# Kernel optimization log

Measured on AMD Instinct MI355X. Metric: run time of the kernel, lower is better.

Reference implementation:

```python
import jax, jax.numpy as jnp
import numpy as np

KH = KW = 3  # deform conv kernel
EPS = 1e-12  # F.normalize eps


def _deform_sample(img, u, v):
    """Flow-guided deformable sampling: bilinear gather of img at each of the
    9 kernel offsets shifted by the per-pixel flow (u=dx, v=dy).
    img: [B,C,H,W]; u,v: [B,1,H,W] -> returns [B,C,9,H,W]."""
    B, C, H, W = img.shape
    ky, kx = jnp.meshgrid(jnp.arange(KH) - 1, jnp.arange(KW) - 1, indexing='ij')
    ky = ky.reshape(1, 9, 1, 1).astype(img.dtype)
    kx = kx.reshape(1, 9, 1, 1).astype(img.dtype)
    iy = jnp.arange(H, dtype=img.dtype).reshape(1, 1, H, 1)
    ix = jnp.arange(W, dtype=img.dtype).reshape(1, 1, 1, W)
    py = iy + ky + v  # [B,9,H,W]
    px = ix + kx + u
    y0 = jnp.floor(py); x0 = jnp.floor(px)
    wy = py - y0; wx = px - x0  # bilinear weights
    y0i = y0.astype(jnp.int32); x0i = x0.astype(jnp.int32)
    flat = img.reshape(B, C, H * W)

    def gather(yi, xi):
        valid = ((yi >= 0) & (yi < H) & (xi >= 0) & (xi < W)).astype(img.dtype)
        idx = jnp.clip(yi, 0, H - 1) * W + jnp.clip(xi, 0, W - 1)  # [B,9,H,W]
        g = jax.vmap(lambda f, i: jnp.take(f, i.reshape(-1), axis=1))(flat, idx)
        return g.reshape(B, C, 9, H, W) * valid[:, None]

    s = (gather(y0i, x0i) * ((1 - wy) * (1 - wx))[:, None]
         + gather(y0i, x0i + 1) * ((1 - wy) * wx)[:, None]
         + gather(y0i + 1, x0i) * (wy * (1 - wx))[:, None]
         + gather(y0i + 1, x0i + 1) * (wy * wx)[:, None])
    return s


def setup_inputs() -> dict:
    key = jax.random.key(0)
    k1, k2, k3, k4, k5 = jax.random.split(key, 5)
    B, C, H, W = 2, 64, 256, 256
    num_heads = 4
    clone = jax.random.normal(k1, (B, C, H, W), dtype=jnp.float32)
    x = jax.random.normal(k2, (B, C, H * W), dtype=jnp.float32)
    u = jax.random.normal(k3, (B, 1, H, W), dtype=jnp.float32)
    v = jax.random.normal(k4, (B, 1, H, W), dtype=jnp.float32)
    weight = jax.random.normal(k5, (C, C, KH, KW), dtype=jnp.float32) * 0.05
    temperature = jnp.ones((num_heads, 1, 1), dtype=jnp.float32)
    return {"clone": clone, "x": x, "u": u, "v": v,
            "weight": weight, "temperature": temperature}


def reference(clone, x, u, v, weight, temperature):
    # deformable conv: bilinear gather then contract over (in_ch, kernel)
    s = _deform_sample(clone, u, v)                      # [B,C,9,H,W]
    w = weight.reshape(weight.shape[0], weight.shape[1], 9)
    conv = jnp.einsum('bckhw,ock->bohw', s, w)           # [B,C,H,W]
    B, C, H, W = conv.shape
    head = temperature.shape[0]
    kv = conv.reshape(B, head, C // head, H * W)          # k = v = deform output
    q = x.reshape(B, head, C // head, H * W)
    qn = q / jnp.maximum(jnp.linalg.norm(q, axis=-1, keepdims=True), EPS)
    kn = kv / jnp.maximum(jnp.linalg.norm(kv, axis=-1, keepdims=True), EPS)
    attn = jnp.einsum('bhcs,bhds->bhcd', qn, kn) * temperature  # [B,h,c,c]
    attn = jax.nn.softmax(attn, axis=-1)
    out = jnp.einsum('bhcd,bhds->bhcs', attn, kv)
    return out.reshape(B, C, H * W)
```

## Files before the change

### kernel.cpp

```cpp
#include <hip/hip_runtime.h>

typedef __bf16 bf16;
typedef __bf16 bf16x4 __attribute__((ext_vector_type(4)));
typedef __bf16 bf16x8 __attribute__((ext_vector_type(8)));
typedef float  f32x4  __attribute__((ext_vector_type(4)));

#define HH 256
#define WW 256
#define NB 2
#define NC 64
#define NS 65536
#define EX 258
#define NHEAD 4
#define DH 16

#define OFF_CEXT   0ul
#define OFF_KV     17040384ul
#define OFF_WPK    33817600ul
#define OFF_ACC    33891328ul

__global__ void k0w(const float* __restrict__ wgt, bf16* __restrict__ wpk,
                    float* __restrict__ accums) {
    int t = blockIdx.x * 256 + threadIdx.x;
    if (t < 9 * 2 * 4 * 64) {
        int L   = t & 63;
        int mtg = (t >> 6) & 3;
        int kc  = (t >> 8) & 1;
        int tap = t >> 9;
        int o  = mtg * 16 + (L & 15);
        int cb = kc * 32 + (L >> 4) * 8;
        bf16x8 vv;
        #pragma unroll
        for (int j = 0; j < 8; j++)
            vv[j] = (bf16)wgt[(o * 64 + (cb + j)) * 9 + tap];
        *(bf16x8*)(wpk + t * 8) = vv;
    }
    int z = t - 9 * 2 * 4 * 64;
    if (z >= 0 && z < 2304) accums[z] = 0.0f;
}

__global__ __launch_bounds__(256, 2) void k1_conv(const float* __restrict__ clone,
                                                  const bf16* __restrict__ wpk,
                                                  bf16* __restrict__ cext) {
    const int Xt = blockIdx.x;
    const int Yt = blockIdx.y;
    const int b  = blockIdx.z;
    const int t  = threadIdx.x;
    const int L  = t & 63;
    const int wv = t >> 6;
    const int mpair = wv >> 1;
    const int npair = wv & 1;

    extern __shared__ bf16 tile[];

    bf16x8 afrag[2][9][2];
    #pragma unroll
    for (int mt = 0; mt < 2; mt++)
        #pragma unroll
        for (int tap = 0; tap < 9; tap++)
            #pragma unroll
            for (int kc = 0; kc < 2; kc++) {
                int idx = ((tap * 2 + kc) * 4 + (mpair * 2 + mt)) * 64 + L;
                afrag[mt][tap][kc] = *(const bf16x8*)(wpk + idx * 8);
            }

    for (int u = t; u < 2176; u += 256) {
        int xq = u % 17;
        int rc = u / 17;
        int cg = rc & 15;
        int r  = rc >> 4;
        int y  = Yt * 6 - 2 + r;
        int xg0 = Xt * 64 - 4 + xq * 4;
        int c0 = cg * 4;
        f32x4 f[4];
        bool yin = (y >= 0) && (y < HH);
        if (yin && xg0 >= 0 && xg0 + 3 < WW) {
            #pragma unroll
            for (int i = 0; i < 4; i++)
                f[i] = *(const f32x4*)(clone + ((size_t)(b * NC + c0 + i) * HH + y) * WW + xg0);
        } else {
            #pragma unroll
            for (int i = 0; i < 4; i++)
                #pragma unroll
                for (int e = 0; e < 4; e++) {
                    int xg = xg0 + e;
                    f[i][e] = (yin && xg >= 0 && xg < WW)
                            ? clone[((size_t)(b * NC + c0 + i) * HH + y) * WW + xg] : 0.0f;
                }
        }
        #pragma unroll
        for (int e = 0; e < 4; e++) {
            bf16x4 h;
            #pragma unroll
            for (int i = 0; i < 4; i++) h[i] = (bf16)f[i][e];
            *(bf16x4*)(tile + (r * 68 + xq * 4 + e) * 72 + c0) = h;
        }
    }
    __syncthreads();

    const f32x4 zero4 = {0.0f, 0.0f, 0.0f, 0.0f};
    for (int Yi = 0; Yi < 6; Yi++) {
        f32x4 acc[2][2];
        acc[0][0] = zero4; acc[0][1] = zero4; acc[1][0] = zero4; acc[1][1] = zero4;
        #pragma unroll
        for (int tap = 0; tap < 9; tap++) {
            const int ky = tap / 3 - 1;
            const int kx = tap % 3 - 1;
            const int r = Yi + 1 + ky;
            #pragma unroll
            for (int kc = 0; kc < 2; kc++) {
                const int cb = kc * 32 + (L >> 4) * 8;
                #pragma unroll
                for (int nt = 0; nt < 2; nt++) {
                    const int col = npair * 32 + nt * 16 + (L & 15) + kx + 3;
                    bf16x8 bfrag = *(const bf16x8*)(tile + (r * 68 + col) * 72 + cb);
                    #pragma unroll
                    for (int mt = 0; mt < 2; mt++)
                        acc[mt][nt] = __builtin_amdgcn_mfma_f32_16x16x32_bf16(
                            afrag[mt][tap][kc], bfrag, acc[mt][nt], 0, 0, 0);
                }
            }
        }
        int Yp = Yt * 6 + Yi;
        #pragma unroll
        for (int mt = 0; mt < 2; mt++)
            #pragma unroll
            for (int nt = 0; nt < 2; nt++) {
                int Xp = Xt * 64 + npair * 32 + nt * 16 + (L & 15);
                if (Xp < EX) {
                    int o = mpair * 32 + mt * 16 + (L >> 4) * 4;
                    bf16x4 st;
                    #pragma unroll
                    for (int rg = 0; rg < 4; rg++) st[rg] = (bf16)acc[mt][nt][rg];
                    *(bf16x4*)(cext + ((((size_t)b * EX + Yp) * EX + Xp) << 6) + o) = st;
                }
            }
    }
}

__global__ __launch_bounds__(256) void k2_gather(const float* __restrict__ uu,
                                                 const float* __restrict__ vv,
                                                 const bf16* __restrict__ cext,
                                                 bf16* __restrict__ kv) {
    const int tx = blockIdx.x;
    const int ty = blockIdx.y;
    const int b  = blockIdx.z;
    const int t  = threadIdx.x;
    const int px = t & 31, py = t >> 5;
    const int hw = (ty * 8 + py) * 256 + tx * 32 + px;
    const int idx = b * NS + hw;
    const int hy = hw >> 8;
    const int wx = hw & 255;
    float fv = vv[idx];
    float fu = uu[idx];
    float py_f = (float)hy + fv;
    float px_f = (float)wx + fu;
    float fy = floorf(py_f);
    float fx = floorf(px_f);
    float ay = py_f - fy;
    float ax = px_f - fx;
    int ys = (int)fy + 1;
    int xs = (int)fx + 1;
    float w00 = (1.0f - ay) * (1.0f - ax);
    float w01 = (1.0f - ay) * ax;
    float w10 = ay * (1.0f - ax);
    float w11 = ay * ax;
    bool y0i = (ys >= 0) && (ys < EX);
    bool y1i = (ys + 1 >= 0) && (ys + 1 < EX);
    bool x0i = (xs >= 0) && (xs < EX);
    bool x1i = (xs + 1 >= 0) && (xs + 1 < EX);
    if (!y0i) { w00 = 0.0f; w01 = 0.0f; }
    if (!y1i) { w10 = 0.0f; w11 = 0.0f; }
    if (!x0i) { w00 = 0.0f; w10 = 0.0f; }
    if (!x1i) { w01 = 0.0f; w11 = 0.0f; }
    int y0c = ys < 0 ? 0 : (ys > EX - 1 ? EX - 1 : ys);
    int y1c = ys + 1 < 0 ? 0 : (ys + 1 > EX - 1 ? EX - 1 : ys + 1);
    int x0c = xs < 0 ? 0 : (xs > EX - 1 ? EX - 1 : xs);
    int x1c = xs + 1 < 0 ? 0 : (xs + 1 > EX - 1 ? EX - 1 : xs + 1);
    const bf16* pb = cext + (((size_t)b * EX * EX) << 6);
    size_t i00 = ((size_t)(y0c * EX + x0c)) << 6;
    size_t i01 = ((size_t)(y0c * EX + x1c)) << 6;
    size_t i10 = ((size_t)(y1c * EX + x0c)) << 6;
    size_t i11 = ((size_t)(y1c * EX + x1c)) << 6;
    bf16* kvp = kv + (((size_t)(b * NC)) << 16) + hw;
    #pragma unroll
    for (int ck = 0; ck < 8; ck++) {
        int c0 = ck * 8;
        bf16x8 c00 = *(const bf16x8*)(pb + i00 + c0);
        bf16x8 c01 = *(const bf16x8*)(pb + i01 + c0);
        bf16x8 c10 = *(const bf16x8*)(pb + i10 + c0);
        bf16x8 c11 = *(const bf16x8*)(pb + i11 + c0);
        #pragma unroll
        for (int j = 0; j < 8; j++) {
            float val = w00 * (float)c00[j] + w01 * (float)c01[j]
                      + w10 * (float)c10[j] + w11 * (float)c11[j];
            kvp[((size_t)(c0 + j)) << 16] = (bf16)val;
        }
    }
}

__global__ __launch_bounds__(256) void k3_dots(const float* __restrict__ x,
                                               const bf16* __restrict__ kv,
                                               float* __restrict__ dots,
                                               float* __restrict__ qss,
                                               float* __restrict__ kss) {
    const int ch = blockIdx.x;
    const int h  = blockIdx.y;
    const int b  = blockIdx.z;
    const int t  = threadIdx.x;
    const int L  = t & 63;
    const int wv = t >> 6;
    const int row = L & 15;
    const int kg  = L >> 4;
    const float* qb = x + ((size_t)(b * NC + h * DH + row)) * NS;
    const bf16*  kb = kv + (((size_t)(b * NC + h * DH + row)) << 16);
    f32x4 acc = {0.0f, 0.0f, 0.0f, 0.0f};
    float qp = 0.0f, kp = 0.0f;
    const int s0 = ch * 512 + wv * 128 + kg * 8;
    #pragma unroll
    for (int it = 0; it < 4; it++) {
        int s = s0 + it * 32;
        f32x4 q0 = *(const f32x4*)(qb + s);
        f32x4 q1 = *(const f32x4*)(qb + s + 4);
        bf16x8 ka = *(const bf16x8*)(kb + s);
        bf16x8 qa;
        #pragma unroll
        for (int j = 0; j < 4; j++) {
            qa[j]     = (bf16)q0[j];
            qa[j + 4] = (bf16)q1[j];
        }
        qp += q0[0]*q0[0] + q0[1]*q0[1] + q0[2]*q0[2] + q0[3]*q0[3]
            + q1[0]*q1[0] + q1[1]*q1[1] + q1[2]*q1[2] + q1[3]*q1[3];
        #pragma unroll
        for (int j = 0; j < 8; j++) {
            float kf = (float)ka[j];
            kp += kf * kf;
        }
        acc = __builtin_amdgcn_mfma_f32_16x16x32_bf16(qa, ka, acc, 0, 0, 0);
    }
    __shared__ float ldsD[256];
    __shared__ float ldsQ[16];
    __shared__ float ldsK[16];
    ldsD[t] = 0.0f;
    if (t < 16) { ldsQ[t] = 0.0f; ldsK[t] = 0.0f; }
    __syncthreads();
    #pragma unroll
    for (int rg = 0; rg < 4; rg++)
        atomicAdd(&ldsD[(kg * 4 + rg) * 16 + row], acc[rg]);
    atomicAdd(&ldsQ[row], qp);
    atomicAdd(&ldsK[row], kp);
    __syncthreads();
    const int bh = b * NHEAD + h;
    atomicAdd(&dots[bh * 256 + t], ldsD[t]);
    if (t < 16) {
        atomicAdd(&qss[bh * 16 + t], ldsQ[t]);
        atomicAdd(&kss[bh * 16 + t], ldsK[t]);
    }
}

__global__ __launch_bounds__(256) void k5_out(const bf16* __restrict__ kv,
                                              const float* __restrict__ dots,
                                              const float* __restrict__ qss,
                                              const float* __restrict__ kss,
                                              const float* __restrict__ temp,
                                              float* __restrict__ out) {
    const int ci = blockIdx.x;
    const int h  = blockIdx.y;
    const int b  = blockIdx.z;
    const int t  = threadIdx.x;
    const int bh = b * NHEAD + h;
    __shared__ float l[256];
    __shared__ float a[256];
    {
        int i = t >> 4, j = t & 15;
        float qn = fmaxf(sqrtf(qss[bh * 16 + i]), 1e-12f);
        float kn = fmaxf(sqrtf(kss[bh * 16 + j]), 1e-12f);
        float logit = dots[bh * 256 + t] / (qn * kn) * temp[h];
        l[t] = logit;
        __syncthreads();
        float mx = -1e30f;
        #pragma unroll
        for (int jj = 0; jj < 16; jj++) mx = fmaxf(mx, l[i * 16 + jj]);
        float sum = 0.0f;
        #pragma unroll
        for (int jj = 0; jj < 16; jj++) sum += expf(l[i * 16 + jj] - mx);
        a[t] = expf(logit - mx) / sum;
        __syncthreads();
    }
    const int s = (ci * 256 + t) * 4;
    const bf16* kvb = kv + (((size_t)(b * NC + h * DH)) << 16) + s;
    f32x4 kf[16];
    #pragma unroll
    for (int j = 0; j < 16; j++) {
        bf16x4 kk = *(const bf16x4*)(kvb + ((size_t)j << 16));
        #pragma unroll
        for (int e = 0; e < 4; e++) kf[j][e] = (float)kk[e];
    }
    float* ob = out + ((size_t)(b * NC + h * DH)) * NS + s;
    #pragma unroll
    for (int i = 0; i < 16; i++) {
        f32x4 o = {0.0f, 0.0f, 0.0f, 0.0f};
        #pragma unroll
        for (int j = 0; j < 16; j++)
            o += a[i * 16 + j] * kf[j];
        *(f32x4*)(ob + (size_t)i * NS) = o;
    }
}

extern "C" void kernel_launch(void* const* d_in, const int* in_sizes, int n_in,
                              void* d_out, int out_size, void* d_ws, size_t ws_size,
                              hipStream_t stream) {
    const float* clone = (const float*)d_in[0];
    const float* x     = (const float*)d_in[1];
    const float* u     = (const float*)d_in[2];
    const float* v     = (const float*)d_in[3];
    const float* wgt   = (const float*)d_in[4];
    const float* temp  = (const float*)d_in[5];
    float* out = (float*)d_out;

    char* ws = (char*)d_ws;
    bf16*  cext   = (bf16*) (ws + OFF_CEXT);
    bf16*  kv     = (bf16*) (ws + OFF_KV);
    bf16*  wpk    = (bf16*) (ws + OFF_WPK);
    float* accums = (float*)(ws + OFF_ACC);
    float* dots = accums;
    float* qss  = accums + 2048;
    float* kss  = accums + 2048 + 128;

    static bool attr_set = false;
    if (!attr_set) {
        hipFuncSetAttribute((const void*)k1_conv,
                            hipFuncAttributeMaxDynamicSharedMemorySize, 78336);
        attr_set = true;
    }

    k0w<<<27, 256, 0, stream>>>(wgt, wpk, accums);
    k1_conv<<<dim3(5, 43, 2), 256, 78336, stream>>>(clone, wpk, cext);
    k2_gather<<<dim3(8, 32, 2), 256, 0, stream>>>(u, v, cext, kv);
    k3_dots<<<dim3(128, 4, 2), 256, 0, stream>>>(x, kv, dots, qss, kss);
    k5_out<<<dim3(64, 4, 2), 256, 0, stream>>>(kv, dots, qss, kss, temp, out);
}
```

Before: 161.7 us.

## Fuse deform gather with q·k dot reduction and stripe global accumulators

Merges the gather kernel and the dots kernel. Each block computes 128 pixels of kv, keeps them in a shared tile and runs the per-head q·k MFMA reduction directly from it, so the separate k3 pass no longer re-reads kv from global memory. Global atomics are spread over 8 accumulator stripes to reduce contention, and k5 sums the stripes. The conv kernel also skips MFMAs for column tiles that lie entirely past the valid extent. In exchange it adds more global atomics per block, since the LDS pre-reduction is gone, and the LDS tile read uses a strided pattern.

```diff
diff --git a/kernel.cpp b/kernel.cpp
--- a/kernel.cpp
+++ b/kernel.cpp
@@ -13,6 +13,8 @@
 #define EX 258
 #define NHEAD 4
 #define DH 16
+#define NSTRIPE 8
+#define ACCSZ 2304
 
 #define OFF_CEXT   0ul
 #define OFF_KV     17040384ul
@@ -36,7 +38,7 @@
         *(bf16x8*)(wpk + t * 8) = vv;
     }
     int z = t - 9 * 2 * 4 * 64;
-    if (z >= 0 && z < 2304) accums[z] = 0.0f;
+    if (z >= 0 && z < NSTRIPE * ACCSZ) accums[z] = 0.0f;
 }
 
 __global__ __launch_bounds__(256, 2) void k1_conv(const float* __restrict__ clone,
@@ -98,6 +100,7 @@
     }
     __syncthreads();
 
+    const int nbase = Xt * 64 + npair * 32;
     const f32x4 zero4 = {0.0f, 0.0f, 0.0f, 0.0f};
     for (int Yi = 0; Yi < 6; Yi++) {
         f32x4 acc[2][2];
@@ -112,12 +115,14 @@
                 const int cb = kc * 32 + (L >> 4) * 8;
                 #pragma unroll
                 for (int nt = 0; nt < 2; nt++) {
-                    const int col = npair * 32 + nt * 16 + (L & 15) + kx + 3;
-                    bf16x8 bfrag = *(const bf16x8*)(tile + (r * 68 + col) * 72 + cb);
-                    #pragma unroll
-                    for (int mt = 0; mt < 2; mt++)
-                        acc[mt][nt] = __builtin_amdgcn_mfma_f32_16x16x32_bf16(
-                            afrag[mt][tap][kc], bfrag, acc[mt][nt], 0, 0, 0);
+                    if (nbase + nt * 16 < EX) {
+                        const int col = npair * 32 + nt * 16 + (L & 15) + kx + 3;
+                        bf16x8 bfrag = *(const bf16x8*)(tile + (r * 68 + col) * 72 + cb);
+                        #pragma unroll
+                        for (int mt = 0; mt < 2; mt++)
+                            acc[mt][nt] = __builtin_amdgcn_mfma_f32_16x16x32_bf16(
+                                afrag[mt][tap][kc], bfrag, acc[mt][nt], 0, 0, 0);
+                    }
                 }
             }
         }
@@ -138,19 +143,25 @@
     }
 }
 
-__global__ __launch_bounds__(256) void k2_gather(const float* __restrict__ uu,
-                                                 const float* __restrict__ vv,
-                                                 const bf16* __restrict__ cext,
-                                                 bf16* __restrict__ kv) {
-    const int tx = blockIdx.x;
-    const int ty = blockIdx.y;
+__global__ __launch_bounds__(256) void k2_gd(const float* __restrict__ uu,
+                                             const float* __restrict__ vv,
+                                             const float* __restrict__ x,
+                                             const bf16* __restrict__ cext,
+                                             bf16* __restrict__ kv,
+                                             float* __restrict__ accums) {
+    const int bx = blockIdx.x;
     const int b  = blockIdx.z;
-    const int t  = threadIdx.x;
-    const int px = t & 31, py = t >> 5;
-    const int hw = (ty * 8 + py) * 256 + tx * 32 + px;
+    const int strip = (bx & 7) * 64 + (bx >> 3);
+    const int t = threadIdx.x;
+    const int px = t >> 1;
+    const int half = t & 1;
+    const int hw = strip * 128 + px;
     const int idx = b * NS + hw;
     const int hy = hw >> 8;
     const int wx = hw & 255;
+
+    __shared__ bf16 tile[128][68];
+
     float fv = vv[idx];
     float fu = uu[idx];
     float py_f = (float)hy + fv;
@@ -182,53 +193,50 @@
     size_t i01 = ((size_t)(y0c * EX + x1c)) << 6;
     size_t i10 = ((size_t)(y1c * EX + x0c)) << 6;
     size_t i11 = ((size_t)(y1c * EX + x1c)) << 6;
-    bf16* kvp = kv + (((size_t)(b * NC)) << 16) + hw;
-    #pragma unroll
-    for (int ck = 0; ck < 8; ck++) {
-        int c0 = ck * 8;
-        bf16x8 c00 = *(const bf16x8*)(pb + i00 + c0);
-        bf16x8 c01 = *(const bf16x8*)(pb + i01 + c0);
-        bf16x8 c10 = *(const bf16x8*)(pb + i10 + c0);
-        bf16x8 c11 = *(const bf16x8*)(pb + i11 + c0);
+    const int c0 = half * 32;
+    bf16* kvp = kv + (((size_t)(b * NC + c0)) << 16) + hw;
+    #pragma unroll
+    for (int g = 0; g < 4; g++) {
+        int cg = c0 + g * 8;
+        bf16x8 c00 = *(const bf16x8*)(pb + i00 + cg);
+        bf16x8 c01 = *(const bf16x8*)(pb + i01 + cg);
+        bf16x8 c10 = *(const bf16x8*)(pb + i10 + cg);
+        bf16x8 c11 = *(const bf16x8*)(pb + i11 + cg);
+        bf16x4 lo, hi;
         #pragma unroll
         for (int j = 0; j < 8; j++) {
             float val = w00 * (float)c00[j] + w01 * (float)c01[j]
                       + w10 * (float)c10[j] + w11 * (float)c11[j];
-            kvp[((size_t)(c0 + j)) << 16] = (bf16)val;
-        }
-    }
-}
-
-__global__ __launch_bounds__(256) void k3_dots(const float* __restrict__ x,
-                                               const bf16* __restrict__ kv,
-                                               float* __restrict__ dots,
-                                               float* __restrict__ qss,
-                                               float* __restrict__ kss) {
-    const int ch = blockIdx.x;
-    const int h  = blockIdx.y;
-    const int b  = blockIdx.z;
-    const int t  = threadIdx.x;
+            bf16 hv = (bf16)val;
+            if (j < 4) lo[j] = hv; else hi[j - 4] = hv;
+            kvp[((size_t)(g * 8 + j)) << 16] = hv;
+        }
+        *(bf16x4*)(&tile[px][c0 + g * 8])     = lo;
+        *(bf16x4*)(&tile[px][c0 + g * 8 + 4]) = hi;
+    }
+    __syncthreads();
+
     const int L  = t & 63;
-    const int wv = t >> 6;
+    const int h  = t >> 6;
     const int row = L & 15;
     const int kg  = L >> 4;
-    const float* qb = x + ((size_t)(b * NC + h * DH + row)) * NS;
-    const bf16*  kb = kv + (((size_t)(b * NC + h * DH + row)) << 16);
+    const int bh = b * NHEAD + h;
+    const float* qb = x + ((size_t)(b * NC + h * DH + row)) * NS + strip * 128;
     f32x4 acc = {0.0f, 0.0f, 0.0f, 0.0f};
     float qp = 0.0f, kp = 0.0f;
-    const int s0 = ch * 512 + wv * 128 + kg * 8;
     #pragma unroll
     for (int it = 0; it < 4; it++) {
-        int s = s0 + it * 32;
+        const int s = it * 32 + kg * 8;
         f32x4 q0 = *(const f32x4*)(qb + s);
         f32x4 q1 = *(const f32x4*)(qb + s + 4);
-        bf16x8 ka = *(const bf16x8*)(kb + s);
-        bf16x8 qa;
+        bf16x8 qa, ka;
         #pragma unroll
         for (int j = 0; j < 4; j++) {
             qa[j]     = (bf16)q0[j];
             qa[j + 4] = (bf16)q1[j];
         }
+        #pragma unroll
+        for (int j = 0; j < 8; j++) ka[j] = tile[s + j][h * DH + row];
         qp += q0[0]*q0[0] + q0[1]*q0[1] + q0[2]*q0[2] + q0[3]*q0[3]
             + q1[0]*q1[0] + q1[1]*q1[1] + q1[2]*q1[2] + q1[3]*q1[3];
         #pragma unroll
@@ -238,30 +246,20 @@
         }
         acc = __builtin_amdgcn_mfma_f32_16x16x32_bf16(qa, ka, acc, 0, 0, 0);
     }
-    __shared__ float ldsD[256];
-    __shared__ float ldsQ[16];
-    __shared__ float ldsK[16];
-    ldsD[t] = 0.0f;
-    if (t < 16) { ldsQ[t] = 0.0f; ldsK[t] = 0.0f; }
-    __syncthreads();
+    float* astripe = accums + (bx & 7) * ACCSZ;
     #pragma unroll
     for (int rg = 0; rg < 4; rg++)
-        atomicAdd(&ldsD[(kg * 4 + rg) * 16 + row], acc[rg]);
-    atomicAdd(&ldsQ[row], qp);
-    atomicAdd(&ldsK[row], kp);
-    __syncthreads();
-    const int bh = b * NHEAD + h;
-    atomicAdd(&dots[bh * 256 + t], ldsD[t]);
-    if (t < 16) {
-        atomicAdd(&qss[bh * 16 + t], ldsQ[t]);
-        atomicAdd(&kss[bh * 16 + t], ldsK[t]);
+        atomicAdd(astripe + bh * 256 + (kg * 4 + rg) * 16 + row, acc[rg]);
+    qp += __shfl_xor(qp, 16); qp += __shfl_xor(qp, 32);
+    kp += __shfl_xor(kp, 16); kp += __shfl_xor(kp, 32);
+    if (kg == 0) {
+        atomicAdd(astripe + 2048 + bh * 16 + row, qp);
+        atomicAdd(astripe + 2176 + bh * 16 + row, kp);
     }
 }
 
 __global__ __launch_bounds__(256) void k5_out(const bf16* __restrict__ kv,
-                                              const float* __restrict__ dots,
-                                              const float* __restrict__ qss,
-                                              const float* __restrict__ kss,
+                                              const float* __restrict__ accums,
                                               const float* __restrict__ temp,
                                               float* __restrict__ out) {
     const int ci = blockIdx.x;
@@ -273,9 +271,16 @@
     __shared__ float a[256];
     {
         int i = t >> 4, j = t & 15;
-        float qn = fmaxf(sqrtf(qss[bh * 16 + i]), 1e-12f);
-        float kn = fmaxf(sqrtf(kss[bh * 16 + j]), 1e-12f);
-        float logit = dots[bh * 256 + t] / (qn * kn) * temp[h];
+        float dsum = 0.0f, q2 = 0.0f, k2 = 0.0f;
+        #pragma unroll
+        for (int st = 0; st < NSTRIPE; st++) {
+            dsum += accums[st * ACCSZ + bh * 256 + t];
+            q2   += accums[st * ACCSZ + 2048 + bh * 16 + i];
+            k2   += accums[st * ACCSZ + 2176 + bh * 16 + j];
+        }
+        float qn = fmaxf(sqrtf(q2), 1e-12f);
+        float kn = fmaxf(sqrtf(k2), 1e-12f);
+        float logit = dsum / (qn * kn) * temp[h];
         l[t] = logit;
         __syncthreads();
         float mx = -1e30f;
@@ -323,9 +328,6 @@
     bf16*  kv     = (bf16*) (ws + OFF_KV);
     bf16*  wpk    = (bf16*) (ws + OFF_WPK);
     float* accums = (float*)(ws + OFF_ACC);
-    float* dots = accums;
-    float* qss  = accums + 2048;
-    float* kss  = accums + 2048 + 128;
 
     static bool attr_set = false;
     if (!attr_set) {
@@ -334,9 +336,8 @@
         attr_set = true;
     }
 
-    k0w<<<27, 256, 0, stream>>>(wgt, wpk, accums);
+    k0w<<<90, 256, 0, stream>>>(wgt, wpk, accums);
     k1_conv<<<dim3(5, 43, 2), 256, 78336, stream>>>(clone, wpk, cext);
-    k2_gather<<<dim3(8, 32, 2), 256, 0, stream>>>(u, v, cext, kv);
-    k3_dots<<<dim3(128, 4, 2), 256, 0, stream>>>(x, kv, dots, qss, kss);
-    k5_out<<<dim3(64, 4, 2), 256, 0, stream>>>(kv, dots, qss, kss, temp, out);
-}
+    k2_gd<<<dim3(512, 1, 2), 256, 0, stream>>>(u, v, x, cext, kv, accums);
+    k5_out<<<dim3(64, 4, 2), 256, 0, stream>>>(kv, accums, temp, out);
+}
```

Result: faster. 158.2 us (-2.1%).
